# Kernel optimization log

Hardware: AMD Instinct MI355X
Metric: run time of the kernel (lower is better)

The kernel has to match this reference:

```python
import jax, jax.numpy as jnp
import numpy as np

N_E = 4096
E_DIM = 64
BETA = 0.25


def setup_inputs() -> dict:
    key = jax.random.key(0)
    k1, k2 = jax.random.split(key)
    z = jax.random.normal(k1, (16, E_DIM, 32, 32), dtype=jnp.float32)
    embedding = jax.random.normal(k2, (N_E, E_DIM), dtype=jnp.float32)
    return {"z": z, "embedding": embedding}


def reference(z, embedding):
    # b c h w -> b h w c
    zc = jnp.transpose(z, (0, 2, 3, 1))  # [B,H,W,C]
    B, H, W, C = zc.shape
    zf = zc.reshape(-1, C)  # [N, C]

    # Squared Euclidean distances (argmin is identical to cdist p=2 argmin)
    # d2[n,e] = |z|^2 - 2 z.e + |e|^2
    d2 = (
        jnp.sum(zf * zf, axis=1, keepdims=True)
        - 2.0 * (zf @ embedding.T)
        + jnp.sum(embedding * embedding, axis=1)[None, :]
    )  # [N, n_e]
    idx = jnp.argmin(d2, axis=1)  # [N]

    z_q = embedding[idx].reshape(B, H, W, C)

    # dist_p == 2 losses
    loss_d1 = jnp.mean((jax.lax.stop_gradient(z_q) - zc) ** 2)
    loss_d2 = jnp.mean((z_q - jax.lax.stop_gradient(zc)) ** 2)
    loss = BETA * loss_d1 + loss_d2

    # Straight-through estimator
    z_q = zc + jax.lax.stop_gradient(z_q - zc)

    indices = idx.reshape(B, H, W)
    z_q = jnp.transpose(z_q, (0, 3, 1, 2))  # b h w c -> b c h w
    return z_q, loss, indices
```

## Files before the change

### kernel.cpp

```cpp
#include <hip/hip_runtime.h>

typedef float f32x4 __attribute__((ext_vector_type(4)));
typedef short bf16x8 __attribute__((ext_vector_type(8)));

#define HW_ 1024
#define NE_ 4096
#define CHW_ 65536
#define ZQ_SIZE 1048576
#define LOSS_OFF ZQ_SIZE
#define IDX_OFF (ZQ_SIZE + 1)
#define LOSS_SCALE (1.25f / 1048576.f)
#define EPS_GAP 0.1f

union FragU { unsigned u[4]; bf16x8 v; };

__device__ __forceinline__ unsigned umin_(unsigned a, unsigned b) { return a < b ? a : b; }
__device__ __forceinline__ unsigned umax_(unsigned a, unsigned b) { return a > b ? a : b; }

__device__ __forceinline__ void top2_(unsigned key, unsigned& s1, unsigned& s2) {
    unsigned t;
    asm("v_med3_u32 %0, %1, %2, %3" : "=v"(t) : "v"(key), "v"(s1), "v"(s2));
    s2 = t;
    s1 = umin_(s1, key);
}

__device__ __forceinline__ void split8(const float* v, FragU& hi, FragU& lo) {
#pragma unroll
    for (int p = 0; p < 4; p++) {
        float a = v[2 * p], b = v[2 * p + 1];
        unsigned ua = __float_as_uint(a), ub = __float_as_uint(b);
        hi.u[p] = (ua >> 16) | (ub & 0xFFFF0000u);
        float la = a - __uint_as_float(ua & 0xFFFF0000u);
        float lb = b - __uint_as_float(ub & 0xFFFF0000u);
        lo.u[p] = (__float_as_uint(la) >> 16) | (__float_as_uint(lb) & 0xFFFF0000u);
    }
}

__device__ __forceinline__ void gload_lds16(const void* g, void* l) {
    __builtin_amdgcn_global_load_lds(
        (const __attribute__((address_space(1))) unsigned*)g,
        (__attribute__((address_space(3))) unsigned*)l, 16, 0, 0);
}

__global__ __launch_bounds__(256) void vq_eprep(
        const float* __restrict__ emb, char* __restrict__ efrag,
        float* __restrict__ h_e, float* __restrict__ out) {
    const int bid = blockIdx.x, tid = threadIdx.x;
    if (bid < 128) {
        int u = bid * 256 + tid;
        int l = u & 63, s = (u >> 6) & 1, t = u >> 7;
        int er = t * 16 + (l & 15);
        int c0 = s * 32 + (l >> 4) * 8;
        const float* ep = emb + (size_t)er * 64 + c0;
        float4 ea = *(const float4*)(ep);
        float4 eb = *(const float4*)(ep + 4);
        float v[8];
        v[0] = -ea.x; v[1] = -ea.y; v[2] = -ea.z; v[3] = -ea.w;
        v[4] = -eb.x; v[5] = -eb.y; v[6] = -eb.z; v[7] = -eb.w;
        FragU hi, lo;
        split8(v, hi, lo);
        char* base = efrag + (size_t)t * 4096 + l * 16;
        *(FragU*)(base + s * 1024) = hi;
        *(FragU*)(base + (2 + s) * 1024) = lo;
    } else {
        int t = (bid - 128) * 256 + tid;
        const float4* er = (const float4*)(emb + (size_t)t * 64);
        float s = 0.f;
#pragma unroll
        for (int k = 0; k < 16; k++) {
            float4 e4 = er[k];
            s = fmaf(e4.x, e4.x, s); s = fmaf(e4.y, e4.y, s);
            s = fmaf(e4.z, e4.z, s); s = fmaf(e4.w, e4.w, s);
        }
        h_e[t] = 0.5f * s;
        if (t == 0) out[LOSS_OFF] = 0.f;
    }
}

__global__ __launch_bounds__(512) void vq_mfma(
        const float* __restrict__ z, const char* __restrict__ efrag,
        const float* __restrict__ h_e,
        unsigned* __restrict__ k1q, unsigned* __restrict__ k2q) {
    __shared__ char buf[2][32768];
    __shared__ __attribute__((aligned(16))) float sh_he[512];

    const int tid = threadIdx.x;
    const int lane = tid & 63;
    const int w = tid >> 6;
    const int lrow = lane & 15;
    const int lgrp = lane >> 4;
    const int es = blockIdx.x >> 6;
    const int rb = blockIdx.x & 63;
    const int e0t = es * 32;
    const int rt0 = rb * 16 + w * 2;
    const int b = rb >> 2;

    sh_he[tid] = h_e[es * 512 + tid];

    {
        const char* src = efrag + (size_t)(e0t + w) * 4096 + lane * 16;
        char* dst = buf[0] + w * 4096;
#pragma unroll
        for (int i = 0; i < 4; i++) gload_lds16(src + i * 1024, dst + i * 1024);
    }

    bf16x8 zh[2][2], zl[2][2];
    float hz[2];
#pragma unroll
    for (int r = 0; r < 2; r++) {
        float ss = 0.f;
#pragma unroll
        for (int s = 0; s < 2; s++) {
            const int hw = ((rt0 + r) * 16 + lrow) & 1023;
            const int c0 = s * 32 + lgrp * 8;
            const float* zp = z + (size_t)b * CHW_ + hw;
            float v[8];
#pragma unroll
            for (int j = 0; j < 8; j++) {
                v[j] = zp[(c0 + j) * HW_];
                ss = fmaf(v[j], v[j], ss);
            }
            FragU hi, lo;
            split8(v, hi, lo);
            zh[r][s] = hi.v;
            zl[r][s] = lo.v;
        }
        ss += __shfl_xor(ss, 16);
        ss += __shfl_xor(ss, 32);
        hz[r] = 0.5f * ss;
    }

    unsigned s1k[2] = {~0u, ~0u};
    unsigned s2k[2] = {~0u, ~0u};

    __syncthreads();
    for (int c = 0; c < 4; c++) {
        if (c < 3) {
            const char* src = efrag + (size_t)(e0t + (c + 1) * 8 + w) * 4096
                              + lane * 16;
            char* dst = buf[(c + 1) & 1] + w * 4096;
#pragma unroll
            for (int i = 0; i < 4; i++) gload_lds16(src + i * 1024, dst + i * 1024);
        }

        const char* cb = buf[c & 1] + lane * 16;
#pragma unroll
        for (int j = 0; j < 8; j++) {
            const char* tb = cb + j * 4096;
            bf16x8 ah0 = *(const bf16x8*)(tb);
            bf16x8 ah1 = *(const bf16x8*)(tb + 1024);
            bf16x8 al0 = *(const bf16x8*)(tb + 2048);
            bf16x8 al1 = *(const bf16x8*)(tb + 3072);
            const int etl = c * 8 + j;
            const f32x4 he = *(const f32x4*)&sh_he[etl * 16 + lgrp * 4];

            f32x4 a0 = he + hz[0], a1 = he + hz[1];

            a0 = __builtin_amdgcn_mfma_f32_16x16x32_bf16(ah0, zh[0][0], a0, 0, 0, 0);
            a1 = __builtin_amdgcn_mfma_f32_16x16x32_bf16(ah0, zh[1][0], a1, 0, 0, 0);
            a0 = __builtin_amdgcn_mfma_f32_16x16x32_bf16(ah1, zh[0][1], a0, 0, 0, 0);
            a1 = __builtin_amdgcn_mfma_f32_16x16x32_bf16(ah1, zh[1][1], a1, 0, 0, 0);
            a0 = __builtin_amdgcn_mfma_f32_16x16x32_bf16(al0, zh[0][0], a0, 0, 0, 0);
            a1 = __builtin_amdgcn_mfma_f32_16x16x32_bf16(al0, zh[1][0], a1, 0, 0, 0);
            a0 = __builtin_amdgcn_mfma_f32_16x16x32_bf16(al1, zh[0][1], a0, 0, 0, 0);
            a1 = __builtin_amdgcn_mfma_f32_16x16x32_bf16(al1, zh[1][1], a1, 0, 0, 0);
            a0 = __builtin_amdgcn_mfma_f32_16x16x32_bf16(ah0, zl[0][0], a0, 0, 0, 0);
            a1 = __builtin_amdgcn_mfma_f32_16x16x32_bf16(ah0, zl[1][0], a1, 0, 0, 0);
            a0 = __builtin_amdgcn_mfma_f32_16x16x32_bf16(ah1, zl[0][1], a0, 0, 0, 0);
            a1 = __builtin_amdgcn_mfma_f32_16x16x32_bf16(ah1, zl[1][1], a1, 0, 0, 0);

            const unsigned eb12 = (unsigned)(es * 512 + etl * 16 + lgrp * 4);
#pragma unroll
            for (int rr = 0; rr < 4; rr++) {
                top2_((__float_as_uint(a0[rr]) & 0xFFFFF000u) | (eb12 + rr), s1k[0], s2k[0]);
                top2_((__float_as_uint(a1[rr]) & 0xFFFFF000u) | (eb12 + rr), s1k[1], s2k[1]);
            }
        }
        __syncthreads();
    }

#pragma unroll
    for (int off = 16; off <= 32; off += 16) {
#pragma unroll
        for (int r = 0; r < 2; r++) {
            unsigned o1 = (unsigned)__shfl_xor((int)s1k[r], off);
            unsigned o2 = (unsigned)__shfl_xor((int)s2k[r], off);
            s2k[r] = umin_(umin_(s2k[r], o2), umax_(s1k[r], o1));
            s1k[r] = umin_(s1k[r], o1);
        }
    }

    if (lane < 16) {
        const int base = es * 16384;
#pragma unroll
        for (int r = 0; r < 2; r++) {
            k1q[base + (rt0 + r) * 16 + lane] = s1k[r];
            k2q[base + (rt0 + r) * 16 + lane] = s2k[r];
        }
    }
}

__global__ __launch_bounds__(256) void vq_final(
        const float* __restrict__ z, const float* __restrict__ emb,
        const unsigned* __restrict__ k1q, const unsigned* __restrict__ k2q,
        float* __restrict__ out) {
    int t = blockIdx.x * 256 + threadIdx.x;
    int n = t & 16383;
    int q = t >> 14;

    unsigned m = 0xFFFFFFFFu, s = 0xFFFFFFFFu;
#pragma unroll
    for (int i = 0; i < 8; i++) {
        unsigned a = k1q[i * 16384 + n];
        unsigned b = k2q[i * 16384 + n];
        unsigned hi = umax_(m, a);
        m = umin_(m, a);
        s = umin_(umin_(s, b), hi);
    }

    int idx = (int)(m & 0xFFFu);
    float s1 = __uint_as_float(m & 0xFFFFF000u);
    float s2 = __uint_as_float(s & 0xFFFFF000u);

    int b = n >> 10, hw = n & 1023;
    const float* zp = z + (size_t)b * CHW_ + hw;
    const int cq = q * 16;

    if (s2 - s1 < EPS_GAP) {
        int i2 = (int)(s & 0xFFFu);
        const float* ea = emb + (size_t)idx * 64;
        const float* eb = emb + (size_t)i2 * 64;
        double da = 0.0, db = 0.0;
#pragma unroll 8
        for (int c = 0; c < 64; c++) {
            double zv = (double)zp[c * HW_];
            double xa = (double)ea[c] - zv;
            double xb = (double)eb[c] - zv;
            da = fma(xa, xa, da);
            db = fma(xb, xb, db);
        }
        if (db < da || (db == da && i2 < idx)) idx = i2;
    }

    const float* er = emb + (size_t)idx * 64 + cq;
    float* zq = out + (size_t)b * CHW_ + hw;
    float lsum = 0.f;
#pragma unroll
    for (int j = 0; j < 16; j++) {
        float e = er[j];
        float d = e - zp[(cq + j) * HW_];
        zq[(cq + j) * HW_] = e;
        lsum = fmaf(d, d, lsum);
    }
    if (q == 0) out[IDX_OFF + n] = (float)idx;

#pragma unroll
    for (int off = 32; off; off >>= 1) lsum += __shfl_down(lsum, off);
    if ((threadIdx.x & 63) == 0) atomicAdd(&out[LOSS_OFF], lsum * LOSS_SCALE);
}

extern "C" void kernel_launch(void* const* d_in, const int* in_sizes, int n_in,
                              void* d_out, int out_size, void* d_ws, size_t ws_size,
                              hipStream_t stream) {
    const float* z   = (const float*)d_in[0];
    const float* emb = (const float*)d_in[1];
    float* out = (float*)d_out;
    char* ws = (char*)d_ws;

    char* efrag   = ws;
    float* h_e    = (float*)(ws + 1048576);
    unsigned* k1q = (unsigned*)(ws + 1065024);
    unsigned* k2q = (unsigned*)(ws + 1589312);

    vq_eprep<<<144, 256, 0, stream>>>(emb, efrag, h_e, out);
    vq_mfma <<<512, 512, 0, stream>>>(z, efrag, h_e, k1q, k2q);
    vq_final<<<256, 256, 0, stream>>>(z, emb, k1q, k2q, out);
}
```

Measured before the change: 52.00 us.

## Switch distance GEMM to 32x32x16 MFMA tiles with larger row blocks

After: 50.79 us (median of 2 runs). 1.02x faster.

```diff
diff --git a/kernel.cpp b/kernel.cpp
--- a/kernel.cpp
+++ b/kernel.cpp
@@ -1,6 +1,7 @@
 #include <hip/hip_runtime.h>
 
 typedef float f32x4 __attribute__((ext_vector_type(4)));
+typedef float f32x16 __attribute__((ext_vector_type(16)));
 typedef short bf16x8 __attribute__((ext_vector_type(8)));
 
 #define HW_ 1024
@@ -48,10 +49,10 @@
     const int bid = blockIdx.x, tid = threadIdx.x;
     if (bid < 128) {
         int u = bid * 256 + tid;
-        int l = u & 63, s = (u >> 6) & 1, t = u >> 7;
-        int er = t * 16 + (l & 15);
-        int c0 = s * 32 + (l >> 4) * 8;
-        const float* ep = emb + (size_t)er * 64 + c0;
+        int l = u & 63, ks = (u >> 6) & 3, t = u >> 8;
+        int erow = t * 32 + (l & 31);
+        int k0 = ks * 16 + (l >> 5) * 8;
+        const float* ep = emb + (size_t)erow * 64 + k0;
         float4 ea = *(const float4*)(ep);
         float4 eb = *(const float4*)(ep + 4);
         float v[8];
@@ -59,9 +60,9 @@
         v[4] = -eb.x; v[5] = -eb.y; v[6] = -eb.z; v[7] = -eb.w;
         FragU hi, lo;
         split8(v, hi, lo);
-        char* base = efrag + (size_t)t * 4096 + l * 16;
-        *(FragU*)(base + s * 1024) = hi;
-        *(FragU*)(base + (2 + s) * 1024) = lo;
+        char* base = efrag + (size_t)t * 8192 + ks * 1024 + l * 16;
+        *(FragU*)(base)        = hi;
+        *(FragU*)(base + 4096) = lo;
     } else {
         int t = (bid - 128) * 256 + tid;
         const float4* er = (const float4*)(emb + (size_t)t * 64);
@@ -87,33 +88,34 @@
     const int tid = threadIdx.x;
     const int lane = tid & 63;
     const int w = tid >> 6;
-    const int lrow = lane & 15;
-    const int lgrp = lane >> 4;
-    const int es = blockIdx.x >> 6;
-    const int rb = blockIdx.x & 63;
-    const int e0t = es * 32;
-    const int rt0 = rb * 16 + w * 2;
-    const int b = rb >> 2;
+    const int col = lane & 31;
+    const int kgrp = lane >> 5;
+    const int es = blockIdx.x >> 5;
+    const int rb = blockIdx.x & 31;
+    const int e0t = es * 16;
+    const int b = rb >> 1;
+    const int row0 = rb * 512 + w * 64;
 
     sh_he[tid] = h_e[es * 512 + tid];
 
     {
-        const char* src = efrag + (size_t)(e0t + w) * 4096 + lane * 16;
-        char* dst = buf[0] + w * 4096;
+        const char* src = efrag + (size_t)(e0t + (w >> 1)) * 8192
+                          + (w & 1) * 4096 + lane * 16;
+        char* dst = buf[0] + (w >> 1) * 8192 + (w & 1) * 4096;
 #pragma unroll
         for (int i = 0; i < 4; i++) gload_lds16(src + i * 1024, dst + i * 1024);
     }
 
-    bf16x8 zh[2][2], zl[2][2];
-    float hz[2];
-#pragma unroll
-    for (int r = 0; r < 2; r++) {
+    bf16x8 Zh[2][4], Zl[2][4];
+    float hzv[2];
+#pragma unroll
+    for (int zt = 0; zt < 2; zt++) {
         float ss = 0.f;
-#pragma unroll
-        for (int s = 0; s < 2; s++) {
-            const int hw = ((rt0 + r) * 16 + lrow) & 1023;
-            const int c0 = s * 32 + lgrp * 8;
-            const float* zp = z + (size_t)b * CHW_ + hw;
+        const int hw = ((rb & 1) << 9) + w * 64 + zt * 32 + col;
+        const float* zp = z + (size_t)b * CHW_ + hw;
+#pragma unroll
+        for (int ks = 0; ks < 4; ks++) {
+            const int c0 = ks * 16 + kgrp * 8;
             float v[8];
 #pragma unroll
             for (int j = 0; j < 8; j++) {
@@ -122,12 +124,11 @@
             }
             FragU hi, lo;
             split8(v, hi, lo);
-            zh[r][s] = hi.v;
-            zl[r][s] = lo.v;
-        }
-        ss += __shfl_xor(ss, 16);
+            Zh[zt][ks] = hi.v;
+            Zl[zt][ks] = lo.v;
+        }
         ss += __shfl_xor(ss, 32);
-        hz[r] = 0.5f * ss;
+        hzv[zt] = 0.5f * ss;
     }
 
     unsigned s1k[2] = {~0u, ~0u};
@@ -136,66 +137,80 @@
     __syncthreads();
     for (int c = 0; c < 4; c++) {
         if (c < 3) {
-            const char* src = efrag + (size_t)(e0t + (c + 1) * 8 + w) * 4096
-                              + lane * 16;
-            char* dst = buf[(c + 1) & 1] + w * 4096;
+            const char* src = efrag + (size_t)(e0t + (c + 1) * 4 + (w >> 1)) * 8192
+                              + (w & 1) * 4096 + lane * 16;
+            char* dst = buf[(c + 1) & 1] + (w >> 1) * 8192 + (w & 1) * 4096;
 #pragma unroll
             for (int i = 0; i < 4; i++) gload_lds16(src + i * 1024, dst + i * 1024);
         }
 
-        const char* cb = buf[c & 1] + lane * 16;
-#pragma unroll
-        for (int j = 0; j < 8; j++) {
-            const char* tb = cb + j * 4096;
-            bf16x8 ah0 = *(const bf16x8*)(tb);
-            bf16x8 ah1 = *(const bf16x8*)(tb + 1024);
-            bf16x8 al0 = *(const bf16x8*)(tb + 2048);
-            bf16x8 al1 = *(const bf16x8*)(tb + 3072);
-            const int etl = c * 8 + j;
-            const f32x4 he = *(const f32x4*)&sh_he[etl * 16 + lgrp * 4];
-
-            f32x4 a0 = he + hz[0], a1 = he + hz[1];
-
-            a0 = __builtin_amdgcn_mfma_f32_16x16x32_bf16(ah0, zh[0][0], a0, 0, 0, 0);
-            a1 = __builtin_amdgcn_mfma_f32_16x16x32_bf16(ah0, zh[1][0], a1, 0, 0, 0);
-            a0 = __builtin_amdgcn_mfma_f32_16x16x32_bf16(ah1, zh[0][1], a0, 0, 0, 0);
-            a1 = __builtin_amdgcn_mfma_f32_16x16x32_bf16(ah1, zh[1][1], a1, 0, 0, 0);
-            a0 = __builtin_amdgcn_mfma_f32_16x16x32_bf16(al0, zh[0][0], a0, 0, 0, 0);
-            a1 = __builtin_amdgcn_mfma_f32_16x16x32_bf16(al0, zh[1][0], a1, 0, 0, 0);
-            a0 = __builtin_amdgcn_mfma_f32_16x16x32_bf16(al1, zh[0][1], a0, 0, 0, 0);
-            a1 = __builtin_amdgcn_mfma_f32_16x16x32_bf16(al1, zh[1][1], a1, 0, 0, 0);
-            a0 = __builtin_amdgcn_mfma_f32_16x16x32_bf16(ah0, zl[0][0], a0, 0, 0, 0);
-            a1 = __builtin_amdgcn_mfma_f32_16x16x32_bf16(ah0, zl[1][0], a1, 0, 0, 0);
-            a0 = __builtin_amdgcn_mfma_f32_16x16x32_bf16(ah1, zl[0][1], a0, 0, 0, 0);
-            a1 = __builtin_amdgcn_mfma_f32_16x16x32_bf16(ah1, zl[1][1], a1, 0, 0, 0);
-
-            const unsigned eb12 = (unsigned)(es * 512 + etl * 16 + lgrp * 4);
-#pragma unroll
-            for (int rr = 0; rr < 4; rr++) {
-                top2_((__float_as_uint(a0[rr]) & 0xFFFFF000u) | (eb12 + rr), s1k[0], s2k[0]);
-                top2_((__float_as_uint(a1[rr]) & 0xFFFFF000u) | (eb12 + rr), s1k[1], s2k[1]);
-            }
+#pragma unroll
+        for (int jt = 0; jt < 4; jt++) {
+            const char* tb = buf[c & 1] + jt * 8192 + lane * 16;
+            bf16x8 Ah[4], Al[4];
+#pragma unroll
+            for (int ks = 0; ks < 4; ks++) {
+                Ah[ks] = *(const bf16x8*)(tb + ks * 1024);
+                Al[ks] = *(const bf16x8*)(tb + 4096 + ks * 1024);
+            }
+            const int tloc = c * 4 + jt;
+            f32x4 he[4];
+#pragma unroll
+            for (int rq = 0; rq < 4; rq++)
+                he[rq] = *(const f32x4*)&sh_he[tloc * 32 + 8 * rq + 4 * kgrp];
+
+            f32x16 c0, c1;
+#pragma unroll
+            for (int rq = 0; rq < 4; rq++)
+#pragma unroll
+                for (int rr = 0; rr < 4; rr++) {
+                    c0[rq * 4 + rr] = he[rq][rr] + hzv[0];
+                    c1[rq * 4 + rr] = he[rq][rr] + hzv[1];
+                }
+
+#pragma unroll
+            for (int ks = 0; ks < 4; ks++) {
+                c0 = __builtin_amdgcn_mfma_f32_32x32x16_bf16(Ah[ks], Zh[0][ks], c0, 0, 0, 0);
+                c1 = __builtin_amdgcn_mfma_f32_32x32x16_bf16(Ah[ks], Zh[1][ks], c1, 0, 0, 0);
+            }
+#pragma unroll
+            for (int ks = 0; ks < 4; ks++) {
+                c0 = __builtin_amdgcn_mfma_f32_32x32x16_bf16(Al[ks], Zh[0][ks], c0, 0, 0, 0);
+                c1 = __builtin_amdgcn_mfma_f32_32x32x16_bf16(Al[ks], Zh[1][ks], c1, 0, 0, 0);
+            }
+#pragma unroll
+            for (int ks = 0; ks < 4; ks++) {
+                c0 = __builtin_amdgcn_mfma_f32_32x32x16_bf16(Ah[ks], Zl[0][ks], c0, 0, 0, 0);
+                c1 = __builtin_amdgcn_mfma_f32_32x32x16_bf16(Ah[ks], Zl[1][ks], c1, 0, 0, 0);
+            }
+
+            const unsigned eb = (unsigned)(es * 512 + tloc * 32 + 4 * kgrp);
+#pragma unroll
+            for (int rq = 0; rq < 4; rq++)
+#pragma unroll
+                for (int rr = 0; rr < 4; rr++) {
+                    const unsigned eo = eb + rr + 8 * rq;
+                    top2_((__float_as_uint(c0[rq * 4 + rr]) & 0xFFFFF000u) | eo, s1k[0], s2k[0]);
+                    top2_((__float_as_uint(c1[rq * 4 + rr]) & 0xFFFFF000u) | eo, s1k[1], s2k[1]);
+                }
         }
         __syncthreads();
     }
 
 #pragma unroll
-    for (int off = 16; off <= 32; off += 16) {
+    for (int r = 0; r < 2; r++) {
+        unsigned o1 = (unsigned)__shfl_xor((int)s1k[r], 32);
+        unsigned o2 = (unsigned)__shfl_xor((int)s2k[r], 32);
+        s2k[r] = umin_(umin_(s2k[r], o2), umax_(s1k[r], o1));
+        s1k[r] = umin_(s1k[r], o1);
+    }
+
+    if (lane < 32) {
+        const int base = es * 16384 + row0;
 #pragma unroll
         for (int r = 0; r < 2; r++) {
-            unsigned o1 = (unsigned)__shfl_xor((int)s1k[r], off);
-            unsigned o2 = (unsigned)__shfl_xor((int)s2k[r], off);
-            s2k[r] = umin_(umin_(s2k[r], o2), umax_(s1k[r], o1));
-            s1k[r] = umin_(s1k[r], o1);
-        }
-    }
-
-    if (lane < 16) {
-        const int base = es * 16384;
-#pragma unroll
-        for (int r = 0; r < 2; r++) {
-            k1q[base + (rt0 + r) * 16 + lane] = s1k[r];
-            k2q[base + (rt0 + r) * 16 + lane] = s2k[r];
+            k1q[base + r * 32 + lane] = s1k[r];
+            k2q[base + r * 32 + lane] = s2k[r];
         }
     }
 }
@@ -273,6 +288,6 @@
     unsigned* k2q = (unsigned*)(ws + 1589312);
 
     vq_eprep<<<144, 256, 0, stream>>>(emb, efrag, h_e, out);
-    vq_mfma <<<512, 512, 0, stream>>>(z, efrag, h_e, k1q, k2q);
+    vq_mfma <<<256, 512, 0, stream>>>(z, efrag, h_e, k1q, k2q);
     vq_final<<<256, 256, 0, stream>>>(z, emb, k1q, k2q, out);
 }
```
